# Kernel tuning notes

Measured on AMD Instinct MI355X. Metric: run time of the kernel, lower is better.

## Reference

```python
import jax, jax.numpy as jnp
import numpy as np

N_NODES = 100000
N_EDGES = 1600000
N_EMBED = 48
N_CONVS = 6
N_GRAPHS = 1000
VOCAB = 100


def setup_inputs() -> dict:
    key = jax.random.key(0)
    ks = jax.random.split(key, 20)
    AtomicNum = jax.random.randint(ks[0], (N_NODES,), 0, VOCAB)
    Edge = jax.random.randint(ks[1], (2, N_EDGES), 0, N_NODES)
    graph_id = jnp.sort(jax.random.randint(ks[2], (N_NODES,), 0, N_GRAPHS))
    s = 1.0 / np.sqrt(N_EMBED)
    def lin(k):
        k1, k2 = jax.random.split(k)
        w = jax.random.uniform(k1, (N_EMBED, N_EMBED), jnp.float32, -s, s)
        b = jax.random.uniform(k2, (N_EMBED,), jnp.float32, -s, s)
        return w, b
    def stacked(k):
        ws, bs = zip(*[lin(kk) for kk in jax.random.split(k, N_CONVS)])
        return jnp.stack(ws), jnp.stack(bs)
    emb = jax.random.normal(ks[3], (VOCAB, N_EMBED), jnp.float32)
    msg_w1, msg_b1 = stacked(ks[4])
    msg_w2, msg_b2 = stacked(ks[5])
    upd_w1, upd_b1 = stacked(ks[6])
    upd_w2, upd_b2 = stacked(ks[7])
    ro_w1, ro_b1 = lin(ks[8])
    k1, k2 = jax.random.split(ks[9])
    ro_w2 = jax.random.uniform(k1, (N_EMBED, 1), jnp.float32, -s, s)
    ro_b2 = jax.random.uniform(k2, (1,), jnp.float32, -s, s)
    return dict(AtomicNum=AtomicNum, Edge=Edge, graph_id=graph_id, emb=emb,
                msg_w1=msg_w1, msg_b1=msg_b1, msg_w2=msg_w2, msg_b2=msg_b2,
                upd_w1=upd_w1, upd_b1=upd_b1, upd_w2=upd_w2, upd_b2=upd_b2,
                ro_w1=ro_w1, ro_b1=ro_b1, ro_w2=ro_w2, ro_b2=ro_b2)


def reference(AtomicNum, Edge, graph_id, emb,
              msg_w1, msg_b1, msg_w2, msg_b2,
              upd_w1, upd_b1, upd_w2, upd_b2,
              ro_w1, ro_b1, ro_w2, ro_b2):
    n_nodes = AtomicNum.shape[0]
    src, dst = Edge[0], Edge[1]
    h = emb[AtomicNum]  # [N, d]
    for l in range(N_CONVS):
        # gather endpoint features, elementwise product, message MLP
        x = h[src] * h[dst]                                      # [E, d]
        m = jax.nn.relu(x @ msg_w1[l] + msg_b1[l]) @ msg_w2[l] + msg_b2[l]
        agg = jax.ops.segment_sum(m, dst, num_segments=n_nodes)  # scatter_add
        u = jax.nn.relu(agg @ upd_w1[l] + upd_b1[l]) @ upd_w2[l] + upd_b2[l]
        h = h + u  # residual update
    y = jax.nn.relu(h @ ro_w1 + ro_b1) @ ro_w2 + ro_b2           # [N, 1]
    # per-graph sum readout (== torch.split by Natom + sum per chunk)
    out = jax.ops.segment_sum(y[:, 0], graph_id, num_segments=N_GRAPHS)
    return out
```

## Files before the change

### kernel.cpp

```cpp
#include <hip/hip_runtime.h>
#include <hip/hip_bf16.h>


#define NE 48
#define NB_SH 8

typedef __attribute__((ext_vector_type(8))) short short8;
typedef __attribute__((ext_vector_type(4))) float floatx4;

__device__ __forceinline__ unsigned short bf16_rne(float v) {
    unsigned u = __float_as_uint(v);
    u += 0x7FFFu + ((u >> 16) & 1u);
    return (unsigned short)(u >> 16);
}

__device__ __forceinline__ void split8p(const float* __restrict__ x, short8& hi, short8& lo) {
    union { unsigned u[4]; short8 s; } H, L;
#pragma unroll
    for (int i = 0; i < 4; ++i) {
        float a = x[2 * i], b = x[2 * i + 1];
        __hip_bfloat162 h2 = __float22bfloat162_rn(make_float2(a, b));
        unsigned h = *reinterpret_cast<unsigned*>(&h2);
        float ra = a - __uint_as_float(h << 16);
        float rb = b - __uint_as_float(h & 0xFFFF0000u);
        __hip_bfloat162 l2 = __float22bfloat162_rn(make_float2(ra, rb));
        H.u[i] = h;
        L.u[i] = *reinterpret_cast<unsigned*>(&l2);
    }
    hi = H.s; lo = L.s;
}

__device__ __forceinline__ void gemm3(const short8& ah0, const short8& al0,
                                      const short8& ah1, const short8& al1,
                                      const short8* __restrict__ hi,
                                      const short8* __restrict__ lo,
                                      int lane, floatx4* acc) {
#pragma unroll
    for (int t = 0; t < 3; ++t) {
        short8 bh0 = hi[(t * 2 + 0) * 64 + lane];
        short8 bh1 = hi[(t * 2 + 1) * 64 + lane];
        short8 bl0 = lo[(t * 2 + 0) * 64 + lane];
        short8 bl1 = lo[(t * 2 + 1) * 64 + lane];
        floatx4 c = {0.0f, 0.0f, 0.0f, 0.0f};
        c = __builtin_amdgcn_mfma_f32_16x16x32_bf16(ah0, bh0, c, 0, 0, 0);
        c = __builtin_amdgcn_mfma_f32_16x16x32_bf16(ah1, bh1, c, 0, 0, 0);
        c = __builtin_amdgcn_mfma_f32_16x16x32_bf16(al0, bh0, c, 0, 0, 0);
        c = __builtin_amdgcn_mfma_f32_16x16x32_bf16(al1, bh1, c, 0, 0, 0);
        c = __builtin_amdgcn_mfma_f32_16x16x32_bf16(ah0, bl0, c, 0, 0, 0);
        c = __builtin_amdgcn_mfma_f32_16x16x32_bf16(ah1, bl1, c, 0, 0, 0);
        acc[t] = c;
    }
}

__global__ __launch_bounds__(256) void embed_kernel(const int* __restrict__ an,
                                                    const float* __restrict__ emb,
                                                    float* __restrict__ h, int n4) {
    int i = blockIdx.x * 256 + threadIdx.x;
    if (i >= n4) return;
    int n = i / 12, q = i - n * 12;
    ((float4*)h)[i] = ((const float4*)emb)[an[n] * 12 + q];
}

__global__ __launch_bounds__(256) void hist_kernel(const int* __restrict__ dst,
                                                   int* __restrict__ cnt, int E) {
    int e = blockIdx.x * 256 + threadIdx.x;
    if (e < E) atomicAdd(&cnt[dst[e]], 1);
}

__global__ __launch_bounds__(256) void scansum_kernel(const int* __restrict__ cnt,
                                                      int* __restrict__ bsum, int N) {
    __shared__ int sw[4];
    const int tid = threadIdx.x, lane = tid & 63, wid = tid >> 6;
    int base = blockIdx.x * 1024;
    int v = 0;
#pragma unroll
    for (int k = 0; k < 4; ++k) {
        int i = base + k * 256 + tid;
        v += (i < N) ? cnt[i] : 0;
    }
#pragma unroll
    for (int o = 1; o < 64; o <<= 1) v += __shfl_xor(v, o, 64);
    if (lane == 0) sw[wid] = v;
    __syncthreads();
    if (tid == 0) bsum[blockIdx.x] = sw[0] + sw[1] + sw[2] + sw[3];
}

__global__ __launch_bounds__(256) void scanb_kernel(int* __restrict__ bsum, int nblk) {
    __shared__ int s[256];
    int tid = threadIdx.x;
    s[tid] = (tid < nblk) ? bsum[tid] : 0;
    __syncthreads();
    if (tid == 0) {
        int run = 0;
        for (int i = 0; i < nblk; ++i) { int t = s[i]; s[i] = run; run += t; }
    }
    __syncthreads();
    if (tid < nblk) bsum[tid] = s[tid];
}

__global__ __launch_bounds__(1024) void scanfix_kernel(const int* __restrict__ cnt,
                                                       const int* __restrict__ bsum,
                                                       int* __restrict__ offs,
                                                       int* __restrict__ gpos, int N) {
    __shared__ int swave[16];
    const int tid = threadIdx.x, lane = tid & 63, wid = tid >> 6;
    int i = blockIdx.x * 1024 + tid;
    int orig = (i < N) ? cnt[i] : 0;
    int v = orig;
#pragma unroll
    for (int off = 1; off < 64; off <<= 1) {
        int u = __shfl_up(v, off, 64);
        if (lane >= off) v += u;
    }
    if (lane == 63) swave[wid] = v;
    __syncthreads();
    if (wid == 0) {
        int w = (lane < 16) ? swave[lane] : 0;
#pragma unroll
        for (int off = 1; off < 16; off <<= 1) {
            int u = __shfl_up(w, off, 64);
            if (lane >= off) w += u;
        }
        if (lane < 16) swave[lane] = w;
    }
    __syncthreads();
    int prefix = (wid > 0) ? swave[wid - 1] : 0;
    int val = bsum[blockIdx.x] + prefix + v - orig;
    if (i < N) {
        offs[i] = val;
        if ((i & 255) == 0) gpos[i >> 8] = val;
    }
}

__global__ __launch_bounds__(256) void partA_kernel(const int* __restrict__ src,
                                                    const int* __restrict__ dst,
                                                    int* __restrict__ gpos,
                                                    int2* __restrict__ pairbuf,
                                                    int E, int NB) {
    __shared__ int lhist[512];
    __shared__ int lbase[512];
    const int tid = threadIdx.x;
    for (int i = tid; i < NB; i += 256) lhist[i] = 0;
    __syncthreads();
    const int base = blockIdx.x * 2048;
    int ssrc[8], sdst[8], rnk[8];
#pragma unroll
    for (int k = 0; k < 8; ++k) {
        int e = base + k * 256 + tid;
        if (e < E) {
            ssrc[k] = src[e]; sdst[k] = dst[e];
            rnk[k] = atomicAdd(&lhist[sdst[k] >> NB_SH], 1);
        }
    }
    __syncthreads();
    for (int i = tid; i < NB; i += 256) {
        int c = lhist[i];
        lbase[i] = c ? atomicAdd(&gpos[i], c) : 0;
    }
    __syncthreads();
#pragma unroll
    for (int k = 0; k < 8; ++k) {
        int e = base + k * 256 + tid;
        if (e < E)
            pairbuf[lbase[sdst[k] >> NB_SH] + rnk[k]] = make_int2(ssrc[k], sdst[k]);
    }
}

__global__ __launch_bounds__(256) void partB_kernel(const int2* __restrict__ pairbuf,
                                                    int* __restrict__ offs,
                                                    int* __restrict__ colsrc, int E) {
    int e = blockIdx.x * 256 + threadIdx.x;
    if (e < E) {
        int2 p = pairbuf[e];
        int pos = atomicAdd(&offs[p.y], 1);
        colsrc[pos] = p.x;
    }
}

__global__ __launch_bounds__(256) void pack_all_kernel(const float* __restrict__ w0,
                                                       const float* __restrict__ w1m,
                                                       const float* __restrict__ w2m,
                                                       const float* __restrict__ w3m,
                                                       const float* __restrict__ w4m,
                                                       short8* __restrict__ hi,
                                                       short8* __restrict__ lo) {
    int idx = blockIdx.x * 256 + threadIdx.x;
    if (idx >= 4 * 2304 + 384) return;
    int slot = idx / 2304;
    int rem  = idx - slot * 2304;
    const float* w = (slot == 0) ? w0 : (slot == 1) ? w1m : (slot == 2) ? w2m
                   : (slot == 3) ? w3m : w4m;
    int lane = rem & 63;
    int s = (rem >> 6) & 1;
    int t = (rem >> 7) % 3;
    int l = (rem >> 7) / 3;
    short8 h8, l8;
#pragma unroll
    for (int i = 0; i < 8; ++i) {
        int k = s * 32 + (lane >> 4) * 8 + i;
        int j = t * 16 + (lane & 15);
        float v = (k < NE) ? w[l * NE * NE + k * NE + j] : 0.0f;
        unsigned short hh = bf16_rne(v);
        float hf = __uint_as_float((unsigned)hh << 16);
        unsigned short ll = bf16_rne(v - hf);
        h8[i] = (short)hh;
        l8[i] = (short)ll;
    }
    hi[idx] = h8;
    lo[idx] = l8;
}

__global__ __launch_bounds__(128, 4) void layer_kernel(
    const float* __restrict__ hin,
    const int* __restrict__ colsrc,
    const int* __restrict__ ends,
    const int* __restrict__ cnt,
    float* __restrict__ hout,
    const short8* __restrict__ bhi,
    const short8* __restrict__ blo,
    const float* __restrict__ b1,
    const short8* __restrict__ w2hi, const short8* __restrict__ w2lo, const float* __restrict__ b2,
    const short8* __restrict__ u1hi, const short8* __restrict__ u1lo, const float* __restrict__ ub1,
    const short8* __restrict__ u2hi, const short8* __restrict__ u2lo, const float* __restrict__ ub2,
    int N,
    int final_layer,
    const int* __restrict__ gid,
    const short8* __restrict__ rw1hi, const short8* __restrict__ rw1lo,
    const float* __restrict__ rb1, const float* __restrict__ rw2,
    const float* __restrict__ rb2, float* __restrict__ out)
{
    __shared__ float tile[2][16][52];
    const int tid  = threadIdx.x;
    const int lane = tid & 63;
    const int wid  = tid >> 6;
    const int n0   = blockIdx.x * 32 + wid * 16;
    if (n0 >= N) return;

    const int m  = lane & 15;
    const int kb = lane >> 4;
    float (*mytile)[52] = tile[wid];

    const int mydeg = cnt[n0 + m];
    const int myend = ends[n0 + m];

    short8 bh[6], bl[6];
#pragma unroll
    for (int i = 0; i < 6; ++i) { bh[i] = bhi[i * 64 + lane]; bl[i] = blo[i * 64 + lane]; }
    const float bb0 = b1[m], bb1 = b1[16 + m], bb2 = b1[32 + m];
    const float rbb0 = fmaxf(bb0, 0.0f), rbb1 = fmaxf(bb1, 0.0f), rbb2 = fmaxf(bb2, 0.0f);
    const float rbb_mine = (lane < 16) ? rbb0 : (lane < 32) ? rbb1 : rbb2;

#pragma unroll 1
    for (int nn = 0; nn < 16; ++nn) {
        const int n = n0 + nn;
        const int deg = __shfl(mydeg, nn, 64);
        const int end = __shfl(myend, nn, 64);
        const int beg = end - deg;

        const float* hd = hin + (size_t)n * NE;
        float4 d0a = ((const float4*)(hd + kb * 8))[0];
        float4 d0b = ((const float4*)(hd + kb * 8))[1];
        float4 d1a = make_float4(0, 0, 0, 0), d1b = d1a;
        if (kb < 2) {
            d1a = ((const float4*)(hd + 32 + kb * 8))[0];
            d1b = ((const float4*)(hd + 32 + kb * 8))[1];
        }

        float s0 = 0.0f, s1 = 0.0f, s2 = 0.0f;
        const int ntile = (deg + 15) >> 4;

        for (int it = 0; it < ntile; ++it) {
            const int rem = deg - it * 16;
            int srow = (m < rem) ? colsrc[beg + it * 16 + m] : N;
            const float* hs = hin + (size_t)srow * NE + kb * 8;

            float x0[8], x1[8];
            {
                float4 a0 = ((const float4*)hs)[0];
                float4 a1 = ((const float4*)hs)[1];
                x0[0] = a0.x * d0a.x; x0[1] = a0.y * d0a.y; x0[2] = a0.z * d0a.z; x0[3] = a0.w * d0a.w;
                x0[4] = a1.x * d0b.x; x0[5] = a1.y * d0b.y; x0[6] = a1.z * d0b.z; x0[7] = a1.w * d0b.w;
            }
            if (kb < 2) {
                float4 a0 = ((const float4*)(hs + 32))[0];
                float4 a1 = ((const float4*)(hs + 32))[1];
                x1[0] = a0.x * d1a.x; x1[1] = a0.y * d1a.y; x1[2] = a0.z * d1a.z; x1[3] = a0.w * d1a.w;
                x1[4] = a1.x * d1b.x; x1[5] = a1.y * d1b.y; x1[6] = a1.z * d1b.z; x1[7] = a1.w * d1b.w;
            } else {
#pragma unroll
                for (int i = 0; i < 8; ++i) x1[i] = 0.0f;
            }

            short8 ah0, al0, ah1, al1;
            split8p(x0, ah0, al0);
            split8p(x1, ah1, al1);

#pragma unroll
            for (int t = 0; t < 3; ++t) {
                short8 bh0 = bh[t * 2 + 0], bh1 = bh[t * 2 + 1];
                short8 bl0 = bl[t * 2 + 0], bl1 = bl[t * 2 + 1];
                floatx4 cc = {0.0f, 0.0f, 0.0f, 0.0f};
                cc = __builtin_amdgcn_mfma_f32_16x16x32_bf16(ah0, bh0, cc, 0, 0, 0);
                cc = __builtin_amdgcn_mfma_f32_16x16x32_bf16(ah1, bh1, cc, 0, 0, 0);
                cc = __builtin_amdgcn_mfma_f32_16x16x32_bf16(al0, bh0, cc, 0, 0, 0);
                cc = __builtin_amdgcn_mfma_f32_16x16x32_bf16(al1, bh1, cc, 0, 0, 0);
                cc = __builtin_amdgcn_mfma_f32_16x16x32_bf16(ah0, bl0, cc, 0, 0, 0);
                cc = __builtin_amdgcn_mfma_f32_16x16x32_bf16(ah1, bl1, cc, 0, 0, 0);
                const float bb = (t == 0) ? bb0 : (t == 1) ? bb1 : bb2;
                float ts = 0.0f;
#pragma unroll
                for (int r = 0; r < 4; ++r)
                    ts += fmaxf(cc[r] + bb, 0.0f);
                if (t == 0) s0 += ts; else if (t == 1) s1 += ts; else s2 += ts;
            }
        }

        s0 += __shfl_xor(s0, 16, 64); s0 += __shfl_xor(s0, 32, 64);
        s1 += __shfl_xor(s1, 16, 64); s1 += __shfl_xor(s1, 32, 64);
        s2 += __shfl_xor(s2, 16, 64); s2 += __shfl_xor(s2, 32, 64);

        float t1v = __shfl(s1, lane & 15, 64);
        float t2v = __shfl(s2, lane & 15, 64);
        float val = (lane < 16) ? s0 : (lane < 32) ? t1v : t2v;
        const float npad = (float)(ntile * 16 - deg);
        val = fmaf(-npad, rbb_mine, val);
        if (lane < 48) mytile[nn][lane] = val;
    }
    asm volatile("s_waitcnt lgkmcnt(0)" ::: "memory");

    float c0[8], c1[8];
    {
        const float* row = &mytile[m][0];
        *(float4*)(c0)     = *(const float4*)(row + kb * 8);
        *(float4*)(c0 + 4) = *(const float4*)(row + kb * 8 + 4);
        if (kb < 2) {
            *(float4*)(c1)     = *(const float4*)(row + 32 + kb * 8);
            *(float4*)(c1 + 4) = *(const float4*)(row + 32 + kb * 8 + 4);
        } else {
#pragma unroll
            for (int i = 0; i < 8; ++i) c1[i] = 0.0f;
        }
    }
    asm volatile("s_waitcnt lgkmcnt(0)" ::: "memory");
    short8 ah0, al0, ah1, al1;
    split8p(c0, ah0, al0);
    split8p(c1, ah1, al1);

    floatx4 acc[3];
    gemm3(ah0, al0, ah1, al1, w2hi, w2lo, lane, acc);

    {
        float b2j[3];
#pragma unroll
        for (int t = 0; t < 3; ++t) b2j[t] = b2[t * 16 + m];
#pragma unroll
        for (int r = 0; r < 4; ++r) {
            float fd = (float)__shfl(mydeg, kb * 4 + r, 64);
#pragma unroll
            for (int t = 0; t < 3; ++t) acc[t][r] = fmaf(fd, b2j[t], acc[t][r]);
        }
    }

#pragma unroll
    for (int t = 0; t < 3; ++t)
#pragma unroll
        for (int r = 0; r < 4; ++r)
            mytile[kb * 4 + r][t * 16 + m] = acc[t][r];
    asm volatile("s_waitcnt lgkmcnt(0)" ::: "memory");
    {
        const float* row = &mytile[m][0];
        *(float4*)(c0)     = *(const float4*)(row + kb * 8);
        *(float4*)(c0 + 4) = *(const float4*)(row + kb * 8 + 4);
        if (kb < 2) {
            *(float4*)(c1)     = *(const float4*)(row + 32 + kb * 8);
            *(float4*)(c1 + 4) = *(const float4*)(row + 32 + kb * 8 + 4);
        } else {
#pragma unroll
            for (int i = 0; i < 8; ++i) c1[i] = 0.0f;
        }
    }
    asm volatile("s_waitcnt lgkmcnt(0)" ::: "memory");
    split8p(c0, ah0, al0);
    split8p(c1, ah1, al1);
    gemm3(ah0, al0, ah1, al1, u1hi, u1lo, lane, acc);
    {
        float bj[3];
#pragma unroll
        for (int t = 0; t < 3; ++t) bj[t] = ub1[t * 16 + m];
#pragma unroll
        for (int t = 0; t < 3; ++t)
#pragma unroll
            for (int r = 0; r < 4; ++r)
                acc[t][r] = fmaxf(acc[t][r] + bj[t], 0.0f);
    }

#pragma unroll
    for (int t = 0; t < 3; ++t)
#pragma unroll
        for (int r = 0; r < 4; ++r)
            mytile[kb * 4 + r][t * 16 + m] = acc[t][r];
    asm volatile("s_waitcnt lgkmcnt(0)" ::: "memory");
    {
        const float* row = &mytile[m][0];
        *(float4*)(c0)     = *(const float4*)(row + kb * 8);
        *(float4*)(c0 + 4) = *(const float4*)(row + kb * 8 + 4);
        if (kb < 2) {
            *(float4*)(c1)     = *(const float4*)(row + 32 + kb * 8);
            *(float4*)(c1 + 4) = *(const float4*)(row + 32 + kb * 8 + 4);
        } else {
#pragma unroll
            for (int i = 0; i < 8; ++i) c1[i] = 0.0f;
        }
    }
    asm volatile("s_waitcnt lgkmcnt(0)" ::: "memory");
    split8p(c0, ah0, al0);
    split8p(c1, ah1, al1);
    gemm3(ah0, al0, ah1, al1, u2hi, u2lo, lane, acc);

    {
        float bj[3];
#pragma unroll
        for (int t = 0; t < 3; ++t) bj[t] = ub2[t * 16 + m];
#pragma unroll
        for (int r = 0; r < 4; ++r) {
            const size_t row = (size_t)(n0 + kb * 4 + r) * NE;
#pragma unroll
            for (int t = 0; t < 3; ++t)
                acc[t][r] += hin[row + t * 16 + m] + bj[t];
        }
    }

    if (!final_layer) {
#pragma unroll
        for (int r = 0; r < 4; ++r) {
            const size_t row = (size_t)(n0 + kb * 4 + r) * NE;
#pragma unroll
            for (int t = 0; t < 3; ++t)
                hout[row + t * 16 + m] = acc[t][r];
        }
        return;
    }

#pragma unroll
    for (int t = 0; t < 3; ++t)
#pragma unroll
        for (int r = 0; r < 4; ++r)
            mytile[kb * 4 + r][t * 16 + m] = acc[t][r];
    asm volatile("s_waitcnt lgkmcnt(0)" ::: "memory");
    {
        const float* row = &mytile[m][0];
        *(float4*)(c0)     = *(const float4*)(row + kb * 8);
        *(float4*)(c0 + 4) = *(const float4*)(row + kb * 8 + 4);
        if (kb < 2) {
            *(float4*)(c1)     = *(const float4*)(row + 32 + kb * 8);
            *(float4*)(c1 + 4) = *(const float4*)(row + 32 + kb * 8 + 4);
        } else {
#pragma unroll
            for (int i = 0; i < 8; ++i) c1[i] = 0.0f;
        }
    }
    split8p(c0, ah0, al0);
    split8p(c1, ah1, al1);
    gemm3(ah0, al0, ah1, al1, rw1hi, rw1lo, lane, acc);

    float p[4] = {0.0f, 0.0f, 0.0f, 0.0f};
    {
        float bj[3], wj[3];
#pragma unroll
        for (int t = 0; t < 3; ++t) { bj[t] = rb1[t * 16 + m]; wj[t] = rw2[t * 16 + m]; }
#pragma unroll
        for (int t = 0; t < 3; ++t)
#pragma unroll
            for (int r = 0; r < 4; ++r)
                p[r] = fmaf(fmaxf(acc[t][r] + bj[t], 0.0f), wj[t], p[r]);
    }
#pragma unroll
    for (int o = 1; o < 16; o <<= 1) {
#pragma unroll
        for (int r = 0; r < 4; ++r) p[r] += __shfl_xor(p[r], o, 16);
    }
    if (m == 0) {
        float b2v = rb2[0];
#pragma unroll
        for (int r = 0; r < 4; ++r) {
            int n = n0 + kb * 4 + r;
            atomicAdd(out + gid[n], p[r] + b2v);
        }
    }
}

extern "C" void kernel_launch(void* const* d_in, const int* in_sizes, int n_in,
                              void* d_out, int out_size, void* d_ws, size_t ws_size,
                              hipStream_t stream) {
    const int*   AtomicNum = (const int*)  d_in[0];
    const int*   Edge      = (const int*)  d_in[1];
    const int*   graph_id  = (const int*)  d_in[2];
    const float* emb       = (const float*)d_in[3];
    const float* msg_w1    = (const float*)d_in[4];
    const float* msg_b1    = (const float*)d_in[5];
    const float* msg_w2    = (const float*)d_in[6];
    const float* msg_b2    = (const float*)d_in[7];
    const float* upd_w1    = (const float*)d_in[8];
    const float* upd_b1    = (const float*)d_in[9];
    const float* upd_w2    = (const float*)d_in[10];
    const float* upd_b2    = (const float*)d_in[11];
    const float* ro_w1     = (const float*)d_in[12];
    const float* ro_b1     = (const float*)d_in[13];
    const float* ro_w2     = (const float*)d_in[14];
    const float* ro_b2     = (const float*)d_in[15];

    const int N = in_sizes[0];
    const int E = in_sizes[1] / 2;
    const int* src = Edge;
    const int* dst = Edge + E;
    const int NB = (N + 255) >> NB_SH;
    const int NBLK = (N + 1023) / 1024;

    float*  h    = (float*)d_ws;
    float*  h2   = h  + (size_t)(N + 1) * NE;
    int*    cnt  = (int*)(h2 + (size_t)(N + 1) * NE);
    int*    offs = cnt + N;
    int*    colsrc = offs + N;
    short8* whi  = (short8*)(colsrc + E);
    short8* wlo  = whi + (4 * 2304 + 384);
    int*    gpos = (int*)(wlo + (4 * 2304 + 384));
    int*    bsum = gpos + NB;
    int2*   pairbuf = (int2*)h2;

    hipMemsetAsync(d_out, 0, (size_t)out_size * sizeof(float), stream);
    hipMemsetAsync(cnt, 0, (size_t)N * sizeof(int), stream);
    hipMemsetAsync(h  + (size_t)N * NE, 0, NE * sizeof(float), stream);
    hipMemsetAsync(h2 + (size_t)N * NE, 0, NE * sizeof(float), stream);

    int n4 = N * 12;
    embed_kernel<<<(n4 + 255) / 256, 256, 0, stream>>>(AtomicNum, emb, h, n4);

    hist_kernel<<<(E + 255) / 256, 256, 0, stream>>>(dst, cnt, E);
    scansum_kernel<<<NBLK, 256, 0, stream>>>(cnt, bsum, N);
    scanb_kernel<<<1, 256, 0, stream>>>(bsum, NBLK);
    scanfix_kernel<<<NBLK, 1024, 0, stream>>>(cnt, bsum, offs, gpos, N);
    partA_kernel<<<(E + 2047) / 2048, 256, 0, stream>>>(src, dst, gpos, pairbuf, E, NB);
    partB_kernel<<<(E + 255) / 256, 256, 0, stream>>>(pairbuf, offs, colsrc, E);

    pack_all_kernel<<<(4 * 2304 + 384 + 255) / 256, 256, 0, stream>>>(
        msg_w1, msg_w2, upd_w1, upd_w2, ro_w1, whi, wlo);

    const float* hin = h;
    float* hout = h2;
    for (int l = 0; l < 6; ++l) {
        layer_kernel<<<(N + 31) / 32, 128, 0, stream>>>(
            hin, colsrc, offs, cnt, hout,
            whi + 0 * 2304 + (size_t)l * 384, wlo + 0 * 2304 + (size_t)l * 384,
            msg_b1 + (size_t)l * NE,
            whi + 1 * 2304 + (size_t)l * 384, wlo + 1 * 2304 + (size_t)l * 384, msg_b2 + (size_t)l * NE,
            whi + 2 * 2304 + (size_t)l * 384, wlo + 2 * 2304 + (size_t)l * 384, upd_b1 + (size_t)l * NE,
            whi + 3 * 2304 + (size_t)l * 384, wlo + 3 * 2304 + (size_t)l * 384, upd_b2 + (size_t)l * NE,
            N,
            (l == 5) ? 1 : 0,
            graph_id,
            whi + 4 * 2304, wlo + 4 * 2304,
            ro_b1, ro_w2, ro_b2, (float*)d_out);
        const float* tmp = hin; hin = hout; hout = (float*)tmp;
    }
}
```

Before: 832.2 us.

## Pad node features to 64-float stride and stage edge gathers through LDS

Node feature rows are now padded from 48 to 64 floats, so each gathered row is 256-byte aligned. The edge gather is reorganised so four lanes cooperatively load one source row with float4 loads into a shared-memory buffer, which is then re-read in MFMA operand layout. The non-final residual write-out is also routed through LDS so each row is stored as coalesced float4s. The goal is fewer memory transactions for the random gathers, at the cost of extra LDS traffic, added waits and a larger workspace.

After: 841.6 us. No clear change (+1.1%).

```diff
diff --git a/kernel.cpp b/kernel.cpp
--- a/kernel.cpp
+++ b/kernel.cpp
@@ -3,6 +3,7 @@
 
 
 #define NE 48
+#define NEP 64
 #define NB_SH 8
 
 typedef __attribute__((ext_vector_type(8))) short short8;
@@ -58,7 +59,7 @@
     int i = blockIdx.x * 256 + threadIdx.x;
     if (i >= n4) return;
     int n = i / 12, q = i - n * 12;
-    ((float4*)h)[i] = ((const float4*)emb)[an[n] * 12 + q];
+    ((float4*)h)[n * (NEP / 4) + q] = ((const float4*)emb)[an[n] * 12 + q];
 }
 
 __global__ __launch_bounds__(256) void hist_kernel(const int* __restrict__ dst,
@@ -230,6 +231,7 @@
     const float* __restrict__ rb2, float* __restrict__ out)
 {
     __shared__ float tile[2][16][52];
+    __shared__ float xbuf[2][16][52];
     const int tid  = threadIdx.x;
     const int lane = tid & 63;
     const int wid  = tid >> 6;
@@ -238,7 +240,10 @@
 
     const int m  = lane & 15;
     const int kb = lane >> 4;
+    const int ge = lane >> 2;
+    const int go = lane & 3;
     float (*mytile)[52] = tile[wid];
+    float (*myxb)[52]   = xbuf[wid];
 
     const int mydeg = cnt[n0 + m];
     const int myend = ends[n0 + m];
@@ -249,6 +254,12 @@
     const float bb0 = b1[m], bb1 = b1[16 + m], bb2 = b1[32 + m];
     const float rbb0 = fmaxf(bb0, 0.0f), rbb1 = fmaxf(bb1, 0.0f), rbb2 = fmaxf(bb2, 0.0f);
     const float rbb_mine = (lane < 16) ? rbb0 : (lane < 32) ? rbb1 : rbb2;
+
+    {
+        float4 z = make_float4(0, 0, 0, 0);
+        float4* zp = (float4*)&mytile[lane >> 2][(lane & 3) * 12];
+        zp[0] = z; zp[1] = z; zp[2] = z;
+    }
 
 #pragma unroll 1
     for (int nn = 0; nn < 16; ++nn) {
@@ -257,7 +268,7 @@
         const int end = __shfl(myend, nn, 64);
         const int beg = end - deg;
 
-        const float* hd = hin + (size_t)n * NE;
+        const float* hd = hin + (size_t)n * NEP;
         float4 d0a = ((const float4*)(hd + kb * 8))[0];
         float4 d0b = ((const float4*)(hd + kb * 8))[1];
         float4 d1a = make_float4(0, 0, 0, 0), d1b = d1a;
@@ -271,21 +282,29 @@
 
         for (int it = 0; it < ntile; ++it) {
             const int rem = deg - it * 16;
-            int srow = (m < rem) ? colsrc[beg + it * 16 + m] : N;
-            const float* hs = hin + (size_t)srow * NE + kb * 8;
+            const int srow = (ge < rem) ? colsrc[beg + it * 16 + ge] : N;
+            const float4* rp = (const float4*)(hin + (size_t)srow * NEP) + go;
+            float4 g0 = rp[0];
+            float4 g1 = rp[4];
+            float4 g2 = rp[8];
+            float* xbp = &myxb[ge][0];
+            *(float4*)(xbp + go * 4)      = g0;
+            *(float4*)(xbp + 16 + go * 4) = g1;
+            *(float4*)(xbp + 32 + go * 4) = g2;
+            asm volatile("s_waitcnt lgkmcnt(0)" ::: "memory");
+
+            const float* xr = &myxb[m][0];
+            float4 a0 = *(const float4*)(xr + kb * 8);
+            float4 a1 = *(const float4*)(xr + kb * 8 + 4);
 
             float x0[8], x1[8];
-            {
-                float4 a0 = ((const float4*)hs)[0];
-                float4 a1 = ((const float4*)hs)[1];
-                x0[0] = a0.x * d0a.x; x0[1] = a0.y * d0a.y; x0[2] = a0.z * d0a.z; x0[3] = a0.w * d0a.w;
-                x0[4] = a1.x * d0b.x; x0[5] = a1.y * d0b.y; x0[6] = a1.z * d0b.z; x0[7] = a1.w * d0b.w;
-            }
+            x0[0] = a0.x * d0a.x; x0[1] = a0.y * d0a.y; x0[2] = a0.z * d0a.z; x0[3] = a0.w * d0a.w;
+            x0[4] = a1.x * d0b.x; x0[5] = a1.y * d0b.y; x0[6] = a1.z * d0b.z; x0[7] = a1.w * d0b.w;
             if (kb < 2) {
-                float4 a0 = ((const float4*)(hs + 32))[0];
-                float4 a1 = ((const float4*)(hs + 32))[1];
-                x1[0] = a0.x * d1a.x; x1[1] = a0.y * d1a.y; x1[2] = a0.z * d1a.z; x1[3] = a0.w * d1a.w;
-                x1[4] = a1.x * d1b.x; x1[5] = a1.y * d1b.y; x1[6] = a1.z * d1b.z; x1[7] = a1.w * d1b.w;
+                float4 a2 = *(const float4*)(xr + 32 + kb * 8);
+                float4 a3 = *(const float4*)(xr + 32 + kb * 8 + 4);
+                x1[0] = a2.x * d1a.x; x1[1] = a2.y * d1a.y; x1[2] = a2.z * d1a.z; x1[3] = a2.w * d1a.w;
+                x1[4] = a3.x * d1b.x; x1[5] = a3.y * d1b.y; x1[6] = a3.z * d1b.z; x1[7] = a3.w * d1b.w;
             } else {
 #pragma unroll
                 for (int i = 0; i < 8; ++i) x1[i] = 0.0f;
@@ -417,28 +436,41 @@
     split8p(c1, ah1, al1);
     gemm3(ah0, al0, ah1, al1, u2hi, u2lo, lane, acc);
 
+    if (!final_layer) {
+#pragma unroll
+        for (int t = 0; t < 3; ++t)
+#pragma unroll
+            for (int r = 0; r < 4; ++r)
+                mytile[kb * 4 + r][t * 16 + m] = acc[t][r];
+        asm volatile("s_waitcnt lgkmcnt(0)" ::: "memory");
+        const float* hrow = hin + (size_t)(n0 + ge) * NEP;
+        float*       orow = hout + (size_t)(n0 + ge) * NEP;
+#pragma unroll
+        for (int j = 0; j < 3; ++j) {
+            float4 bv = *(const float4*)(ub2 + j * 16 + go * 4);
+            float4 rv = *(const float4*)(hrow + j * 16 + go * 4);
+            float4 av = *(const float4*)(&mytile[ge][j * 16 + go * 4]);
+            float4 ov;
+            ov.x = rv.x + av.x + bv.x;
+            ov.y = rv.y + av.y + bv.y;
+            ov.z = rv.z + av.z + bv.z;
+            ov.w = rv.w + av.w + bv.w;
+            *(float4*)(orow + j * 16 + go * 4) = ov;
+        }
+        return;
+    }
+
     {
         float bj[3];
 #pragma unroll
         for (int t = 0; t < 3; ++t) bj[t] = ub2[t * 16 + m];
 #pragma unroll
         for (int r = 0; r < 4; ++r) {
-            const size_t row = (size_t)(n0 + kb * 4 + r) * NE;
+            const size_t row = (size_t)(n0 + kb * 4 + r) * NEP;
 #pragma unroll
             for (int t = 0; t < 3; ++t)
                 acc[t][r] += hin[row + t * 16 + m] + bj[t];
         }
-    }
-
-    if (!final_layer) {
-#pragma unroll
-        for (int r = 0; r < 4; ++r) {
-            const size_t row = (size_t)(n0 + kb * 4 + r) * NE;
-#pragma unroll
-            for (int t = 0; t < 3; ++t)
-                hout[row + t * 16 + m] = acc[t][r];
-        }
-        return;
     }
 
 #pragma unroll
@@ -517,8 +549,8 @@
     const int NBLK = (N + 1023) / 1024;
 
     float*  h    = (float*)d_ws;
-    float*  h2   = h  + (size_t)(N + 1) * NE;
-    int*    cnt  = (int*)(h2 + (size_t)(N + 1) * NE);
+    float*  h2   = h  + (size_t)(N + 1) * NEP;
+    int*    cnt  = (int*)(h2 + (size_t)(N + 1) * NEP);
     int*    offs = cnt + N;
     int*    colsrc = offs + N;
     short8* whi  = (short8*)(colsrc + E);
@@ -529,8 +561,8 @@
 
     hipMemsetAsync(d_out, 0, (size_t)out_size * sizeof(float), stream);
     hipMemsetAsync(cnt, 0, (size_t)N * sizeof(int), stream);
-    hipMemsetAsync(h  + (size_t)N * NE, 0, NE * sizeof(float), stream);
-    hipMemsetAsync(h2 + (size_t)N * NE, 0, NE * sizeof(float), stream);
+    hipMemsetAsync(h  + (size_t)N * NEP, 0, NEP * sizeof(float), stream);
+    hipMemsetAsync(h2 + (size_t)N * NEP, 0, NEP * sizeof(float), stream);
 
     int n4 = N * 12;
     embed_kernel<<<(n4 + 255) / 256, 256, 0, stream>>>(AtomicNum, emb, h, n4);
```

## Fold msg_w2 into upd_w1 algebraically and stage update weights in LDS

Applied to the files above, without the earlier changes.

Segment-sum is linear, so (sum m) @ U1 equals (sum relu-part) @ (W2·U1) + deg·(b2·U1). A new fold kernel precomputes W2·U1 and b2·U1 per layer, which removes one 48x48 GEMM plus one tile round trip per node in every layer. The per-layer folded and update weights are also copied into shared memory at block start. This adds a preprocessing kernel, a block-wide barrier and extra LDS use, and the fold changes floating-point rounding order.

Measured after the change: 1.033 ms. +24.1%, slower.

```diff
diff --git a/kernel.cpp b/kernel.cpp
--- a/kernel.cpp
+++ b/kernel.cpp
@@ -32,8 +32,8 @@
 
 __device__ __forceinline__ void gemm3(const short8& ah0, const short8& al0,
                                       const short8& ah1, const short8& al1,
-                                      const short8* __restrict__ hi,
-                                      const short8* __restrict__ lo,
+                                      const short8* hi,
+                                      const short8* lo,
                                       int lane, floatx4* acc) {
 #pragma unroll
     for (int t = 0; t < 3; ++t) {
@@ -61,6 +61,34 @@
     ((float4*)h)[i] = ((const float4*)emb)[an[n] * 12 + q];
 }
 
+__global__ __launch_bounds__(256) void fold_kernel(const float* __restrict__ w2,
+                                                   const float* __restrict__ u1,
+                                                   const float* __restrict__ b2,
+                                                   float* __restrict__ F,
+                                                   float* __restrict__ b2u1) {
+    int idx = blockIdx.x * 256 + threadIdx.x;
+    if (idx < 6 * NE * NE) {
+        int l = idx / (NE * NE);
+        int r = idx - l * NE * NE;
+        int k = r / NE, j = r - (r / NE) * NE;
+        const float* wrow = w2 + (size_t)l * NE * NE + k * NE;
+        const float* ucol = u1 + (size_t)l * NE * NE + j;
+        float s = 0.0f;
+#pragma unroll 8
+        for (int q = 0; q < NE; ++q) s = fmaf(wrow[q], ucol[q * NE], s);
+        F[idx] = s;
+    } else if (idx < 6 * NE * NE + 6 * NE) {
+        int r = idx - 6 * NE * NE;
+        int l = r / NE, j = r - l * NE;
+        const float* bv = b2 + (size_t)l * NE;
+        const float* ucol = u1 + (size_t)l * NE * NE + j;
+        float s = 0.0f;
+#pragma unroll 8
+        for (int q = 0; q < NE; ++q) s = fmaf(bv[q], ucol[q * NE], s);
+        b2u1[r] = s;
+    }
+}
+
 __global__ __launch_bounds__(256) void hist_kernel(const int* __restrict__ dst,
                                                    int* __restrict__ cnt, int E) {
     int e = blockIdx.x * 256 + threadIdx.x;
@@ -181,15 +209,13 @@
                                                        const float* __restrict__ w1m,
                                                        const float* __restrict__ w2m,
                                                        const float* __restrict__ w3m,
-                                                       const float* __restrict__ w4m,
                                                        short8* __restrict__ hi,
                                                        short8* __restrict__ lo) {
     int idx = blockIdx.x * 256 + threadIdx.x;
-    if (idx >= 4 * 2304 + 384) return;
+    if (idx >= 3 * 2304 + 384) return;
     int slot = idx / 2304;
     int rem  = idx - slot * 2304;
-    const float* w = (slot == 0) ? w0 : (slot == 1) ? w1m : (slot == 2) ? w2m
-                   : (slot == 3) ? w3m : w4m;
+    const float* w = (slot == 0) ? w0 : (slot == 1) ? w1m : (slot == 2) ? w2m : w3m;
     int lane = rem & 63;
     int s = (rem >> 6) & 1;
     int t = (rem >> 7) % 3;
@@ -219,9 +245,11 @@
     const short8* __restrict__ bhi,
     const short8* __restrict__ blo,
     const float* __restrict__ b1,
-    const short8* __restrict__ w2hi, const short8* __restrict__ w2lo, const float* __restrict__ b2,
-    const short8* __restrict__ u1hi, const short8* __restrict__ u1lo, const float* __restrict__ ub1,
-    const short8* __restrict__ u2hi, const short8* __restrict__ u2lo, const float* __restrict__ ub2,
+    const short8* __restrict__ f1hi, const short8* __restrict__ f1lo,
+    const float* __restrict__ b2u1v,
+    const float* __restrict__ ub1,
+    const short8* __restrict__ u2hi, const short8* __restrict__ u2lo,
+    const float* __restrict__ ub2,
     int N,
     int final_layer,
     const int* __restrict__ gid,
@@ -230,10 +258,24 @@
     const float* __restrict__ rb2, float* __restrict__ out)
 {
     __shared__ float tile[2][16][52];
+    __shared__ short8 wlds[2][2][384];
     const int tid  = threadIdx.x;
     const int lane = tid & 63;
     const int wid  = tid >> 6;
-    const int n0   = blockIdx.x * 32 + wid * 16;
+
+    for (int i = tid; i < 1536; i += 128) {
+        int mat = i >> 9;
+        int mm  = i / 768;
+        int r   = i - mm * 768;
+        int hl  = r / 384;
+        int f   = r - hl * 384;
+        const short8* src = (mm == 0) ? (hl ? f1lo : f1hi) : (hl ? u2lo : u2hi);
+        wlds[mm][hl][f] = src[f];
+        (void)mat;
+    }
+    __syncthreads();
+
+    const int n0 = blockIdx.x * 32 + wid * 16;
     if (n0 >= N) return;
 
     const int m  = lane & 15;
@@ -347,17 +389,17 @@
     split8p(c1, ah1, al1);
 
     floatx4 acc[3];
-    gemm3(ah0, al0, ah1, al1, w2hi, w2lo, lane, acc);
-
+    gemm3(ah0, al0, ah1, al1, &wlds[0][0][0], &wlds[0][1][0], lane, acc);
     {
-        float b2j[3];
-#pragma unroll
-        for (int t = 0; t < 3; ++t) b2j[t] = b2[t * 16 + m];
+        float dj[3], bj[3];
+#pragma unroll
+        for (int t = 0; t < 3; ++t) { dj[t] = b2u1v[t * 16 + m]; bj[t] = ub1[t * 16 + m]; }
 #pragma unroll
         for (int r = 0; r < 4; ++r) {
             float fd = (float)__shfl(mydeg, kb * 4 + r, 64);
 #pragma unroll
-            for (int t = 0; t < 3; ++t) acc[t][r] = fmaf(fd, b2j[t], acc[t][r]);
+            for (int t = 0; t < 3; ++t)
+                acc[t][r] = fmaxf(fmaf(fd, dj[t], acc[t][r]) + bj[t], 0.0f);
         }
     }
 
@@ -382,40 +424,7 @@
     asm volatile("s_waitcnt lgkmcnt(0)" ::: "memory");
     split8p(c0, ah0, al0);
     split8p(c1, ah1, al1);
-    gemm3(ah0, al0, ah1, al1, u1hi, u1lo, lane, acc);
-    {
-        float bj[3];
-#pragma unroll
-        for (int t = 0; t < 3; ++t) bj[t] = ub1[t * 16 + m];
-#pragma unroll
-        for (int t = 0; t < 3; ++t)
-#pragma unroll
-            for (int r = 0; r < 4; ++r)
-                acc[t][r] = fmaxf(acc[t][r] + bj[t], 0.0f);
-    }
-
-#pragma unroll
-    for (int t = 0; t < 3; ++t)
-#pragma unroll
-        for (int r = 0; r < 4; ++r)
-            mytile[kb * 4 + r][t * 16 + m] = acc[t][r];
-    asm volatile("s_waitcnt lgkmcnt(0)" ::: "memory");
-    {
-        const float* row = &mytile[m][0];
-        *(float4*)(c0)     = *(const float4*)(row + kb * 8);
-        *(float4*)(c0 + 4) = *(const float4*)(row + kb * 8 + 4);
-        if (kb < 2) {
-            *(float4*)(c1)     = *(const float4*)(row + 32 + kb * 8);
-            *(float4*)(c1 + 4) = *(const float4*)(row + 32 + kb * 8 + 4);
-        } else {
-#pragma unroll
-            for (int i = 0; i < 8; ++i) c1[i] = 0.0f;
-        }
-    }
-    asm volatile("s_waitcnt lgkmcnt(0)" ::: "memory");
-    split8p(c0, ah0, al0);
-    split8p(c1, ah1, al1);
-    gemm3(ah0, al0, ah1, al1, u2hi, u2lo, lane, acc);
+    gemm3(ah0, al0, ah1, al1, &wlds[1][0][0], &wlds[1][1][0], lane, acc);
 
     {
         float bj[3];
@@ -522,9 +531,11 @@
     int*    offs = cnt + N;
     int*    colsrc = offs + N;
     short8* whi  = (short8*)(colsrc + E);
-    short8* wlo  = whi + (4 * 2304 + 384);
-    int*    gpos = (int*)(wlo + (4 * 2304 + 384));
+    short8* wlo  = whi + (3 * 2304 + 384);
+    int*    gpos = (int*)(wlo + (3 * 2304 + 384));
     int*    bsum = gpos + NB;
+    float*  foldF = (float*)(bsum + NBLK);
+    float*  b2u1  = foldF + 6 * NE * NE;
     int2*   pairbuf = (int2*)h2;
 
     hipMemsetAsync(d_out, 0, (size_t)out_size * sizeof(float), stream);
@@ -534,6 +545,9 @@
 
     int n4 = N * 12;
     embed_kernel<<<(n4 + 255) / 256, 256, 0, stream>>>(AtomicNum, emb, h, n4);
+
+    fold_kernel<<<(6 * NE * NE + 6 * NE + 255) / 256, 256, 0, stream>>>(
+        msg_w2, upd_w1, msg_b2, foldF, b2u1);
 
     hist_kernel<<<(E + 255) / 256, 256, 0, stream>>>(dst, cnt, E);
     scansum_kernel<<<NBLK, 256, 0, stream>>>(cnt, bsum, N);
@@ -542,8 +556,8 @@
     partA_kernel<<<(E + 2047) / 2048, 256, 0, stream>>>(src, dst, gpos, pairbuf, E, NB);
     partB_kernel<<<(E + 255) / 256, 256, 0, stream>>>(pairbuf, offs, colsrc, E);
 
-    pack_all_kernel<<<(4 * 2304 + 384 + 255) / 256, 256, 0, stream>>>(
-        msg_w1, msg_w2, upd_w1, upd_w2, ro_w1, whi, wlo);
+    pack_all_kernel<<<(3 * 2304 + 384 + 255) / 256, 256, 0, stream>>>(
+        msg_w1, foldF, upd_w2, ro_w1, whi, wlo);
 
     const float* hin = h;
     float* hout = h2;
@@ -552,13 +566,15 @@
             hin, colsrc, offs, cnt, hout,
             whi + 0 * 2304 + (size_t)l * 384, wlo + 0 * 2304 + (size_t)l * 384,
             msg_b1 + (size_t)l * NE,
-            whi + 1 * 2304 + (size_t)l * 384, wlo + 1 * 2304 + (size_t)l * 384, msg_b2 + (size_t)l * NE,
-            whi + 2 * 2304 + (size_t)l * 384, wlo + 2 * 2304 + (size_t)l * 384, upd_b1 + (size_t)l * NE,
-            whi + 3 * 2304 + (size_t)l * 384, wlo + 3 * 2304 + (size_t)l * 384, upd_b2 + (size_t)l * NE,
+            whi + 1 * 2304 + (size_t)l * 384, wlo + 1 * 2304 + (size_t)l * 384,
+            b2u1 + (size_t)l * NE,
+            upd_b1 + (size_t)l * NE,
+            whi + 2 * 2304 + (size_t)l * 384, wlo + 2 * 2304 + (size_t)l * 384,
+            upd_b2 + (size_t)l * NE,
             N,
             (l == 5) ? 1 : 0,
             graph_id,
-            whi + 4 * 2304, wlo + 4 * 2304,
+            whi + 3 * 2304, wlo + 3 * 2304,
             ro_b1, ro_w2, ro_b2, (float*)d_out);
         const float* tmp = hin; hin = hout; hout = (float*)tmp;
     }
```
